# Kernel optimization log

Hardware: AMD Instinct MI355X
Metric: run time of the kernel (lower is better)

## Reference

```python
import jax, jax.numpy as jnp
import numpy as np

RMIN, RMAX, MAX_PHASE = 0.9, 1.0, 6.283


def setup_inputs() -> dict:
    key = jax.random.key(0)
    ks = jax.random.split(key, 12)
    Bsz, T, U, O, S, H = 16, 4096, 128, 128, 256, 512
    inp = jax.random.normal(ks[0], (Bsz, T, U), dtype=jnp.float32)
    # stable complex diagonal: |lambda| in [RMIN, RMAX], phase in [0, MAX_PHASE]
    r = RMIN + (RMAX - RMIN) * jax.random.uniform(ks[1], (S,), dtype=jnp.float32)
    theta = MAX_PHASE * jax.random.uniform(ks[2], (S,), dtype=jnp.float32)
    Lambda_re = r * jnp.cos(theta)
    Lambda_im = r * jnp.sin(theta)
    B = jax.random.normal(ks[3], (S, U), dtype=jnp.float32) / np.sqrt(U)
    C = jax.random.normal(ks[4], (O, S), dtype=jnp.float32) / np.sqrt(S)
    D = jax.random.normal(ks[5], (O, U), dtype=jnp.float32) / np.sqrt(U)
    W1 = jax.random.normal(ks[6], (H, O), dtype=jnp.float32) / np.sqrt(O)
    W2 = jax.random.normal(ks[7], (H, H), dtype=jnp.float32) / np.sqrt(H)
    W3 = jax.random.normal(ks[8], (O, H), dtype=jnp.float32) / np.sqrt(H)
    Wlin = jax.random.normal(ks[9], (O, U), dtype=jnp.float32) / np.sqrt(U)
    return {"input": inp, "Lambda_re": Lambda_re, "Lambda_im": Lambda_im,
            "B": B, "C": C, "D": D, "W1": W1, "W2": W2, "W3": W3, "Wlin": Wlin}


def _linear_scan(lam, bu):
    # lam: (S,) complex; bu: (B, T, S) complex
    # h_t = lam * h_{t-1} + bu_t, h_0 = 0  (work-efficient associative scan)
    A = jnp.broadcast_to(lam[None, None, :], bu.shape)

    def combine(c1, c2):
        a1, x1 = c1
        a2, x2 = c2
        return a1 * a2, a2 * x1 + x2

    _, h = jax.lax.associative_scan(combine, (A, bu), axis=1)
    return h


def reference(input, Lambda_re, Lambda_im, B, C, D, W1, W2, W3, Wlin):
    lam = (Lambda_re + 1j * Lambda_im).astype(jnp.complex64)        # (S,)
    bu = jnp.einsum('btu,su->bts', input, B).astype(jnp.complex64)   # (B,T,S)
    h = _linear_scan(lam, bu)                                        # (B,T,S) complex
    # LRU readout: real(C h) + D u
    y = jnp.einsum('bts,os->bto', h, C.astype(jnp.complex64)).real \
        + jnp.einsum('btu,ou->bto', input, D)                        # (B,T,O)
    # MLP: Linear->SiLU->Linear->ReLU->Linear (no biases)
    z = jax.nn.silu(y @ W1.T)
    z = jax.nn.relu(z @ W2.T)
    mlp_out = z @ W3.T                                               # (B,T,O)
    # residual linear path
    return mlp_out + input @ Wlin.T
```

## Files before the change

### kernel.cpp

```cpp
#include <hip/hip_runtime.h>
#include <hip/hip_bf16.h>

#define BSZ 16
#define TT 4096
#define UU 128
#define OO 128
#define SS 256
#define HH 512
#define BT (BSZ*TT)
#define CLEN 64
#define NCH (TT/CLEN)

using bf16x8 = __attribute__((ext_vector_type(8))) short;
using f32x4  = __attribute__((ext_vector_type(4))) float;

__device__ __forceinline__ unsigned short f2bf(float x){
  union { float f; unsigned int u; } v; v.f = x;
  unsigned int r = v.u + 0x7fffu + ((v.u >> 16) & 1u);
  return (unsigned short)(r >> 16);
}
__device__ __forceinline__ float bf2f(unsigned short h){
  union { float f; unsigned int u; } v; v.u = ((unsigned int)h) << 16;
  return v.f;
}

#define GLD16(g, s) __builtin_amdgcn_global_load_lds( \
    (const __attribute__((address_space(1))) unsigned int*)(g), \
    (__attribute__((address_space(3))) unsigned int*)(s), 16, 0, 0)

#define SBAR() do{ __builtin_amdgcn_sched_barrier(0); \
                   __builtin_amdgcn_s_barrier(); \
                   __builtin_amdgcn_sched_barrier(0); }while(0)

__global__ __launch_bounds__(256) void split_k(const float* __restrict__ x,
                                               unsigned short* __restrict__ H,
                                               unsigned short* __restrict__ L, int n4){
  int i = blockIdx.x * 256 + threadIdx.x;
  if (i >= n4) return;
  float4 v = ((const float4*)x)[i];
  unsigned short h0 = f2bf(v.x), h1 = f2bf(v.y), h2 = f2bf(v.z), h3 = f2bf(v.w);
  ushort4 hh = make_ushort4(h0, h1, h2, h3);
  ushort4 ll = make_ushort4(f2bf(v.x - bf2f(h0)), f2bf(v.y - bf2f(h1)),
                            f2bf(v.z - bf2f(h2)), f2bf(v.w - bf2f(h3)));
  ((ushort4*)H)[i] = hh;
  ((ushort4*)L)[i] = ll;
}

struct WJobs {
  const float* src[7];
  unsigned short* H[7];
  unsigned short* L[7];
  int end4[7];
};
__global__ __launch_bounds__(256) void split_w(WJobs j, int total4){
  int i = blockIdx.x * 256 + threadIdx.x;
  if (i >= total4) return;
  int t = 0, base = 0;
  #pragma unroll
  for (int k = 0; k < 7; k++){
    if (i >= j.end4[k]){ t = k + 1; base = j.end4[k]; }
  }
  int idx = i - base;
  float4 v = ((const float4*)j.src[t])[idx];
  unsigned short h0 = f2bf(v.x), h1 = f2bf(v.y), h2 = f2bf(v.z), h3 = f2bf(v.w);
  ushort4 hh = make_ushort4(h0, h1, h2, h3);
  ushort4 ll = make_ushort4(f2bf(v.x - bf2f(h0)), f2bf(v.y - bf2f(h1)),
                            f2bf(v.z - bf2f(h2)), f2bf(v.w - bf2f(h3)));
  ((ushort4*)j.H[t])[idx] = hh;
  ((ushort4*)j.L[t])[idx] = ll;
}

__global__ __launch_bounds__(256, 2) void gemm_split(
    const unsigned short* __restrict__ AH1, const unsigned short* __restrict__ AL1,
    const unsigned short* __restrict__ BH1, const unsigned short* __restrict__ BL1, int K1, int f1,
    const unsigned short* __restrict__ AH2, const unsigned short* __restrict__ AL2,
    const unsigned short* __restrict__ BH2, const unsigned short* __restrict__ BL2, int K2, int f2,
    unsigned short* __restrict__ outH, unsigned short* __restrict__ outL,
    float* __restrict__ outF, int Nout, int EPI,
    const float* __restrict__ lre, const float* __restrict__ lim,
    float2* __restrict__ ends)
{
  __shared__ __align__(16) unsigned short SM[32768];
  unsigned short* Ah = SM;
  unsigned short* Al = SM + 8192;
  unsigned short* Bh = SM + 16384;
  unsigned short* Bl = SM + 24576;

  const int tid = threadIdx.x;
  const int mb = blockIdx.x, nb = blockIdx.y;
  const int l = tid & 63, w = tid >> 6;
  const int wr = w >> 1, wc = w & 1;
  const int fr = l & 15, fq = l >> 4;

  f32x4 acc[4][4];
  #pragma unroll
  for (int m = 0; m < 4; m++)
    #pragma unroll
    for (int n = 0; n < 4; n++) acc[m][n] = f32x4{0.f, 0.f, 0.f, 0.f};

  const int nkt = (K1 + K2) >> 5;

  auto STAGE = [&](int buf, int kt){
    const int k0 = kt << 5;
    const unsigned short *aH, *aL, *bH, *bL; int st, kk, flg;
    if (k0 < K1){ aH = AH1; aL = AL1; bH = BH1; bL = BL1; st = K1; kk = k0; flg = f1; }
    else        { aH = AH2; aL = AL2; bH = BH2; bL = BL2; st = K2; kk = k0 - K1; flg = f2; }
    #pragma unroll
    for (int it = 0; it < 2; it++){
      int seg = tid + it * 256;
      int r = seg >> 2, c4 = seg & 3;
      int sc = (c4 ^ ((r >> 1) & 3)) << 3;
      size_t go = (size_t)(mb*128 + r) * st + kk + sc;
      size_t gb = (size_t)(nb*128 + r) * st + kk + sc;
      int lo = buf*4096 + r*32 + c4*8;
      GLD16(aH + go, Ah + lo);
      if (flg & 1) GLD16(aL + go, Al + lo);
      GLD16(bH + gb, Bh + lo);
      if (flg & 2) GLD16(bL + gb, Bl + lo);
    }
  };

  STAGE(0, 0);
  __syncthreads();

  for (int kt = 0; kt < nkt; kt++){
    const int cur = kt & 1;
    const int flg = ((kt << 5) < K1) ? f1 : f2;
    if (kt + 1 < nkt) STAGE(cur ^ 1, kt + 1);

    bf16x8 a_h[4], a_l[4], b_h[4], b_l[4];
    #pragma unroll
    for (int m = 0; m < 4; m++){
      int lra = wr*64 + m*16 + fr;
      int ra = cur*4096 + lra*32 + ((fq ^ ((lra >> 1) & 3)) << 3);
      a_h[m] = *(const bf16x8*)&Ah[ra];
      if (flg & 1) a_l[m] = *(const bf16x8*)&Al[ra];
      int lrb = wc*64 + m*16 + fr;
      int rb = cur*4096 + lrb*32 + ((fq ^ ((lrb >> 1) & 3)) << 3);
      b_h[m] = *(const bf16x8*)&Bh[rb];
      if (flg & 2) b_l[m] = *(const bf16x8*)&Bl[rb];
    }
    __builtin_amdgcn_s_setprio(1);
    #pragma unroll
    for (int m = 0; m < 4; m++)
      #pragma unroll
      for (int n = 0; n < 4; n++)
        acc[m][n] = __builtin_amdgcn_mfma_f32_16x16x32_bf16(a_h[m], b_h[n], acc[m][n], 0, 0, 0);
    if (flg & 1)
      #pragma unroll
      for (int m = 0; m < 4; m++)
        #pragma unroll
        for (int n = 0; n < 4; n++)
          acc[m][n] = __builtin_amdgcn_mfma_f32_16x16x32_bf16(a_l[m], b_h[n], acc[m][n], 0, 0, 0);
    if (flg & 2)
      #pragma unroll
      for (int m = 0; m < 4; m++)
        #pragma unroll
        for (int n = 0; n < 4; n++)
          acc[m][n] = __builtin_amdgcn_mfma_f32_16x16x32_bf16(a_h[m], b_l[n], acc[m][n], 0, 0, 0);
    __builtin_amdgcn_s_setprio(0);

    __syncthreads();
  }

  float* fl = (float*)SM;
  #pragma unroll
  for (int m = 0; m < 4; m++)
    #pragma unroll
    for (int n = 0; n < 4; n++)
      #pragma unroll
      for (int j = 0; j < 4; j++)
        fl[(wr*64 + m*16 + fq*4 + j)*128 + wc*64 + n*16 + fr] = acc[m][n][j];
  __syncthreads();
  #pragma unroll
  for (int it = 0; it < 8; it++){
    int task = tid + (it << 8);
    int rl = task >> 4, cg = task & 15;
    float4 v0 = *(const float4*)&fl[rl*128 + cg*8];
    float4 v1 = *(const float4*)&fl[rl*128 + cg*8 + 4];
    size_t o = (size_t)(mb*128 + rl) * Nout + nb*128 + cg*8;
    if (EPI == 0){
      *(float4*)(outF + o)     = v0;
      *(float4*)(outF + o + 4) = v1;
    } else {
      float xv[8] = {v0.x,v0.y,v0.z,v0.w,v1.x,v1.y,v1.z,v1.w};
      union { unsigned short us[8]; uint4 v; } ph, pl;
      #pragma unroll
      for (int e = 0; e < 8; e++){
        float x = xv[e];
        if (EPI == 2)      x = x / (1.f + __expf(-x));
        else if (EPI == 3) x = fmaxf(x, 0.f);
        ph.us[e] = f2bf(x);
        pl.us[e] = f2bf(x - bf2f(ph.us[e]));
      }
      *(uint4*)(outH + o) = ph.v;
      if (outL) *(uint4*)(outL + o) = pl.v;
    }
  }
  if (ends){
    int c = tid >> 7, sl = tid & 127;
    int b = mb >> 5, chunk = ((mb & 31) << 1) + c;
    int s = nb*128 + sl;
    float lr = lre[s], li = lim[s];
    float hr = 0.f, hi2 = 0.f;
    for (int t = 0; t < 64; t++){
      float x = fl[(c*64 + t)*128 + sl];
      float nr = fmaf(lr, hr, fmaf(-li, hi2, x));
      float ni = fmaf(lr, hi2, li * hr);
      hr = nr; hi2 = ni;
    }
    ends[((size_t)(b*NCH + chunk))*SS + s] = make_float2(hr, hi2);
  }
}

#define RING_OFF 65536

__global__ __launch_bounds__(1024, 1) void mlp_fused(
    const unsigned short* __restrict__ yH,
    const unsigned short* __restrict__ W1H,
    const unsigned short* __restrict__ W2H,
    unsigned short* __restrict__ z2H)
{
  __shared__ __align__(16) unsigned char LDS[163840];
  const int tid = threadIdx.x;
  const int l = tid & 63, w = tid >> 6;
  const int fr = l & 15, fq = l >> 4;
  const size_t r0 = (size_t)blockIdx.x * 64;

  const unsigned short* w1base[2];
  const unsigned short* w2base[2];
  int rlds[2];
  #pragma unroll
  for (int it = 0; it < 2; it++){
    int seg = l + (it << 6);
    int r = seg >> 2, c4 = seg & 3;
    int sc = (c4 ^ ((r >> 1) & 3)) << 3;
    w1base[it] = W1H + (size_t)(w*32 + r) * UU + sc;
    w2base[it] = W2H + (size_t)(w*32 + r) * HH + sc;
    rlds[it] = RING_OFF + w*6144 + seg*16;
  }
  auto stageW1 = [&](int kt){
    const int so = (kt % 3) * 2048;
    #pragma unroll
    for (int it = 0; it < 2; it++) GLD16(w1base[it] + kt*32, LDS + rlds[it] + so);
  };
  auto stageW2 = [&](int kt){
    const int so = (kt % 3) * 2048;
    #pragma unroll
    for (int it = 0; it < 2; it++) GLD16(w2base[it] + kt*32, LDS + rlds[it] + so);
  };

  {
    int r = tid >> 4, c16 = tid & 15;
    GLD16(yH + (size_t)(r0 + r) * UU + ((c16 ^ (r & 7)) << 3), LDS + tid*16);
  }
  stageW1(0);
  stageW1(1);
  asm volatile("s_waitcnt vmcnt(4)" ::: "memory");
  SBAR();

  f32x4 acc[4][2];
  #pragma unroll
  for (int m = 0; m < 4; m++)
    #pragma unroll
    for (int n = 0; n < 2; n++) acc[m][n] = f32x4{0.f, 0.f, 0.f, 0.f};

  for (int kt = 0; kt < 4; kt++){
    if (kt < 3) asm volatile("s_waitcnt vmcnt(2)" ::: "memory");
    else        asm volatile("s_waitcnt vmcnt(0)" ::: "memory");
    __builtin_amdgcn_sched_barrier(0);
    const unsigned char* Wb = LDS + RING_OFF + w*6144 + (kt % 3)*2048;
    bf16x8 a[4], b[2];
    #pragma unroll
    for (int m = 0; m < 4; m++){
      int row = m*16 + fr, kc = kt*4 + fq;
      a[m] = *(const bf16x8*)(LDS + (row*128 + ((kc ^ (row & 7)) << 3))*2);
    }
    #pragma unroll
    for (int n = 0; n < 2; n++){
      int rl = n*16 + fr;
      b[n] = *(const bf16x8*)(Wb + rl*64 + ((fq ^ ((rl >> 1) & 3)) << 4));
    }
    __builtin_amdgcn_s_setprio(1);
    #pragma unroll
    for (int m = 0; m < 4; m++)
      #pragma unroll
      for (int n = 0; n < 2; n++)
        acc[m][n] = __builtin_amdgcn_mfma_f32_16x16x32_bf16(a[m], b[n], acc[m][n], 0, 0, 0);
    __builtin_amdgcn_s_setprio(0);
    if (kt + 2 < 4) stageW1(kt + 2);
  }
  SBAR();

  stageW2(0);
  stageW2(1);

  unsigned short* Z1 = (unsigned short*)LDS;
  #pragma unroll
  for (int m = 0; m < 4; m++)
    #pragma unroll
    for (int n = 0; n < 2; n++)
      #pragma unroll
      for (int j = 0; j < 4; j++){
        float x = acc[m][n][j];
        x = x / (1.f + __expf(-x));
        int row = m*16 + fq*4 + j;
        int col = w*32 + n*16 + fr;
        Z1[(col >> 3)*512 + row*8 + (col & 7)] = f2bf(x);
      }
  SBAR();

  #pragma unroll
  for (int m = 0; m < 4; m++)
    #pragma unroll
    for (int n = 0; n < 2; n++) acc[m][n] = f32x4{0.f, 0.f, 0.f, 0.f};

  for (int kt = 0; kt < 16; kt++){
    if (kt < 15) asm volatile("s_waitcnt vmcnt(2)" ::: "memory");
    else         asm volatile("s_waitcnt vmcnt(0)" ::: "memory");
    __builtin_amdgcn_sched_barrier(0);
    const unsigned char* Wb = LDS + RING_OFF + w*6144 + (kt % 3)*2048;
    bf16x8 a[4], b[2];
    #pragma unroll
    for (int m = 0; m < 4; m++)
      a[m] = *(const bf16x8*)(LDS + (size_t)(kt*4 + fq)*1024 + (m*16 + fr)*16);
    #pragma unroll
    for (int n = 0; n < 2; n++){
      int rl = n*16 + fr;
      b[n] = *(const bf16x8*)(Wb + rl*64 + ((fq ^ ((rl >> 1) & 3)) << 4));
    }
    __builtin_amdgcn_s_setprio(1);
    #pragma unroll
    for (int m = 0; m < 4; m++)
      #pragma unroll
      for (int n = 0; n < 2; n++)
        acc[m][n] = __builtin_amdgcn_mfma_f32_16x16x32_bf16(a[m], b[n], acc[m][n], 0, 0, 0);
    __builtin_amdgcn_s_setprio(0);
    if (kt + 2 < 16) stageW2(kt + 2);
  }
  SBAR();

  unsigned short* EP = (unsigned short*)(LDS + RING_OFF);
  #pragma unroll
  for (int m = 0; m < 4; m++)
    #pragma unroll
    for (int n = 0; n < 2; n++)
      #pragma unroll
      for (int j = 0; j < 4; j++){
        float x = fmaxf(acc[m][n][j], 0.f);
        EP[(m*16 + fq*4 + j)*512 + w*32 + n*16 + fr] = f2bf(x);
      }
  __syncthreads();
  #pragma unroll
  for (int it = 0; it < 4; it++){
    int seg = tid + (it << 10);
    int r = seg >> 6, c8 = seg & 63;
    *(uint4*)(z2H + (r0 + r)*HH + c8*8) = *(const uint4*)&EP[r*512 + c8*8];
  }
}

__global__ __launch_bounds__(256) void scan_carries(const float2* __restrict__ ends,
                                                    const float* __restrict__ lre,
                                                    const float* __restrict__ lim,
                                                    float2* __restrict__ carryin){
  const int idx = blockIdx.x * 256 + threadIdx.x;
  const int b = idx >> 8;
  const int s = idx & 255;
  float pr = lre[s], pi = lim[s];
  #pragma unroll
  for (int q = 0; q < 6; q++){
    float nr = pr*pr - pi*pi;
    float ni = 2.f * pr * pi;
    pr = nr; pi = ni;
  }
  float hr = 0.f, hi = 0.f;
  for (int c = 0; c < NCH; c++){
    size_t o = ((size_t)b*NCH + c)*SS + s;
    carryin[o] = make_float2(hr, hi);
    float2 e = ends[o];
    float nr = fmaf(pr, hr, fmaf(-pi, hi, e.x));
    float ni = fmaf(pr, hi, fmaf(pi, hr, e.y));
    hr = nr; hi = ni;
  }
}

__global__ __launch_bounds__(256) void scan_apply_v(
    const unsigned short* __restrict__ buH, const unsigned short* __restrict__ buL,
    const float* __restrict__ lre, const float* __restrict__ lim,
    const float2* __restrict__ carryin, unsigned short* __restrict__ RehH){
  const int tid = threadIdx.x;
  const int grp = tid >> 6, ln = tid & 63;
  const int chunk = blockIdx.x * 4 + grp;
  const int b = chunk >> 6, ch = chunk & 63;
  const int s0 = ln * 4;
  float lr[4], li[4], hr[4], hi[4];
  #pragma unroll
  for (int e = 0; e < 4; e++){ lr[e] = lre[s0+e]; li[e] = lim[s0+e]; }
  const float2* ci = &carryin[((size_t)(b*NCH + ch))*SS + s0];
  #pragma unroll
  for (int e = 0; e < 4; e++){ hr[e] = ci[e].x; hi[e] = ci[e].y; }
  const size_t rbase = ((size_t)b*TT + (size_t)ch*CLEN)*SS + s0;
  for (int t = 0; t < CLEN; t++){
    uint2 hv = *(const uint2*)(buH + rbase + (size_t)t*SS);
    uint2 lv = *(const uint2*)(buL + rbase + (size_t)t*SS);
    const unsigned short* hs = (const unsigned short*)&hv;
    const unsigned short* ls = (const unsigned short*)&lv;
    uint2 ov; unsigned short* os = (unsigned short*)&ov;
    #pragma unroll
    for (int e = 0; e < 4; e++){
      float x = bf2f(hs[e]) + bf2f(ls[e]);
      float nr = fmaf(lr[e], hr[e], fmaf(-li[e], hi[e], x));
      float ni = fmaf(lr[e], hi[e], li[e] * hr[e]);
      hr[e] = nr; hi[e] = ni;
      os[e] = f2bf(nr);
    }
    *(uint2*)(RehH + rbase + (size_t)t*SS) = ov;
  }
}

extern "C" void kernel_launch(void* const* d_in, const int* in_sizes, int n_in,
                              void* d_out, int out_size, void* d_ws, size_t ws_size,
                              hipStream_t stream){
  const float* inp = (const float*)d_in[0];
  const float* lre = (const float*)d_in[1];
  const float* lim = (const float*)d_in[2];
  const float* Bm  = (const float*)d_in[3];
  const float* Cm  = (const float*)d_in[4];
  const float* Dm  = (const float*)d_in[5];
  const float* W1  = (const float*)d_in[6];
  const float* W2  = (const float*)d_in[7];
  const float* W3  = (const float*)d_in[8];
  const float* Wl  = (const float*)d_in[9];
  float* out = (float*)d_out;

  char* ws = (char*)d_ws;
  size_t off = 0;
  auto alloc = [&](size_t bytes)->char*{
    char* p = ws + off; off += (bytes + 255) & ~(size_t)255; return p;
  };
  unsigned short* inH  = (unsigned short*)alloc((size_t)BT*UU*2);
  unsigned short* inL  = (unsigned short*)alloc((size_t)BT*UU*2);
  char* Rbu = alloc((size_t)BT*SS*2*2);
  unsigned short* buH = (unsigned short*)Rbu;
  unsigned short* buL = (unsigned short*)(Rbu + (size_t)BT*SS*2);
  char* R2 = alloc((size_t)BT*HH*2);
  unsigned short* RehH = (unsigned short*)R2;
  unsigned short* yH   = (unsigned short*)(R2 + (size_t)BT*SS*2);
  unsigned short* z2H  = (unsigned short*)Rbu;
  unsigned short* BwH = (unsigned short*)alloc((size_t)SS*UU*2);
  unsigned short* BwL = (unsigned short*)alloc((size_t)SS*UU*2);
  unsigned short* CH_ = (unsigned short*)alloc((size_t)OO*SS*2);
  unsigned short* CL_ = (unsigned short*)alloc((size_t)OO*SS*2);
  unsigned short* DH_ = (unsigned short*)alloc((size_t)OO*UU*2);
  unsigned short* DL_ = (unsigned short*)alloc((size_t)OO*UU*2);
  unsigned short* W1H = (unsigned short*)alloc((size_t)HH*OO*2);
  unsigned short* W1L = (unsigned short*)alloc((size_t)HH*OO*2);
  unsigned short* W2H = (unsigned short*)alloc((size_t)HH*HH*2);
  unsigned short* W2L = (unsigned short*)alloc((size_t)HH*HH*2);
  unsigned short* W3H = (unsigned short*)alloc((size_t)OO*HH*2);
  unsigned short* W3L = (unsigned short*)alloc((size_t)OO*HH*2);
  unsigned short* WlH = (unsigned short*)alloc((size_t)OO*UU*2);
  unsigned short* WlL = (unsigned short*)alloc((size_t)OO*UU*2);
  float2* ends    = (float2*)alloc((size_t)BSZ*NCH*SS*8);
  float2* carryin = (float2*)alloc((size_t)BSZ*NCH*SS*8);
  if (off > ws_size) return;

  split_k<<<(BT*UU/4 + 255)/256, 256, 0, stream>>>(inp, inH, inL, BT*UU/4);
  {
    WJobs j;
    const float* srcs[7] = {Bm, Cm, Dm, W1, W2, W3, Wl};
    unsigned short* Hs[7] = {BwH, CH_, DH_, W1H, W2H, W3H, WlH};
    unsigned short* Ls[7] = {BwL, CL_, DL_, W1L, W2L, W3L, WlL};
    int n4s[7] = {SS*UU/4, OO*SS/4, OO*UU/4, HH*OO/4, HH*HH/4, OO*HH/4, OO*UU/4};
    int cum = 0;
    for (int k = 0; k < 7; k++){
      j.src[k] = srcs[k]; j.H[k] = Hs[k]; j.L[k] = Ls[k];
      cum += n4s[k]; j.end4[k] = cum;
    }
    split_w<<<(cum + 255)/256, 256, 0, stream>>>(j, cum);
  }

  gemm_split<<<dim3(BT/128, SS/128), 256, 0, stream>>>(
      inH, inL, BwH, BwL, UU, 3,
      inH, inL, BwH, BwL, 0,  3,
      buH, buL, nullptr, SS, 1,
      lre, lim, ends);

  scan_carries<<<(BSZ*SS)/256, 256, 0, stream>>>(ends, lre, lim, carryin);

  scan_apply_v<<<BSZ*NCH/4, 256, 0, stream>>>(buH, buL, lre, lim, carryin, RehH);

  gemm_split<<<dim3(BT/128, OO/128), 256, 0, stream>>>(
      RehH, RehH, CH_, CL_, SS, 2,
      inH,  inL,  DH_, DL_, UU, 3,
      yH, nullptr, nullptr, OO, 1,
      nullptr, nullptr, nullptr);

  mlp_fused<<<BT/64, 1024, 0, stream>>>(yH, W1H, W2H, z2H);

  gemm_split<<<dim3(BT/128, OO/128), 256, 0, stream>>>(
      z2H, z2H, W3H, W3L, HH, 2,
      inH, inL, WlH, WlL, UU, 3,
      nullptr, nullptr, out, OO, 0,
      nullptr, nullptr, nullptr);
}
```

Baseline: 204.8 us.

## Fuse W3 output GEMM and residual Wlin path into fused MLP kernel

Extends the fused MLP kernel to also compute the third MLP layer (z2·W3ᵀ with split-bf16 weights) and the residual input·Wlinᵀ (3-term split precision), writing fp32 output directly. This removes the z2 intermediate round trip through global memory (BT×512 bf16 write and read) and one kernel launch. The trade-off is a longer kernel per block with extra weight staging through the LDS ring, more LDS loads of the input tile, and additional barriers.

```diff
diff --git a/kernel.cpp b/kernel.cpp
--- a/kernel.cpp
+++ b/kernel.cpp
@@ -217,45 +217,51 @@
 
 __global__ __launch_bounds__(1024, 1) void mlp_fused(
     const unsigned short* __restrict__ yH,
-    const unsigned short* __restrict__ W1H,
-    const unsigned short* __restrict__ W2H,
-    unsigned short* __restrict__ z2H)
+    const unsigned short* __restrict__ inH, const unsigned short* __restrict__ inL,
+    const unsigned short* __restrict__ W1H, const unsigned short* __restrict__ W2H,
+    const unsigned short* __restrict__ W3H, const unsigned short* __restrict__ W3L,
+    const unsigned short* __restrict__ WlH, const unsigned short* __restrict__ WlL,
+    float* __restrict__ out)
 {
   __shared__ __align__(16) unsigned char LDS[163840];
   const int tid = threadIdx.x;
   const int l = tid & 63, w = tid >> 6;
   const int fr = l & 15, fq = l >> 4;
+  const int mh = w >> 3, nf = w & 7;
   const size_t r0 = (size_t)blockIdx.x * 64;
-
-  const unsigned short* w1base[2];
-  const unsigned short* w2base[2];
-  int rlds[2];
-  #pragma unroll
-  for (int it = 0; it < 2; it++){
-    int seg = l + (it << 6);
-    int r = seg >> 2, c4 = seg & 3;
-    int sc = (c4 ^ ((r >> 1) & 3)) << 3;
-    w1base[it] = W1H + (size_t)(w*32 + r) * UU + sc;
-    w2base[it] = W2H + (size_t)(w*32 + r) * HH + sc;
-    rlds[it] = RING_OFF + w*6144 + seg*16;
-  }
-  auto stageW1 = [&](int kt){
+  const int ringb = RING_OFF + w*6144;
+
+  auto stage32 = [&](const unsigned short* W, int strideK, int kt){
     const int so = (kt % 3) * 2048;
     #pragma unroll
-    for (int it = 0; it < 2; it++) GLD16(w1base[it] + kt*32, LDS + rlds[it] + so);
+    for (int it = 0; it < 2; it++){
+      int seg = l + (it << 6);
+      int r = seg >> 2, c4 = seg & 3;
+      GLD16(W + (size_t)(w*32 + r) * strideK + kt*32 + ((c4 ^ ((r >> 1) & 3)) << 3),
+            LDS + ringb + so + seg*16);
+    }
   };
-  auto stageW2 = [&](int kt){
+  auto stagePair = [&](const unsigned short* PH, const unsigned short* PL, int strideK, int kt){
     const int so = (kt % 3) * 2048;
     #pragma unroll
-    for (int it = 0; it < 2; it++) GLD16(w2base[it] + kt*32, LDS + rlds[it] + so);
+    for (int it = 0; it < 2; it++){
+      int seg = l + (it << 6);
+      const unsigned short* P = (seg >> 6) ? PL : PH;
+      int rr = (seg >> 2) & 15, c4 = seg & 3;
+      GLD16(P + (size_t)(nf*16 + rr) * strideK + kt*32 + ((c4 ^ ((rr >> 1) & 3)) << 3),
+            LDS + ringb + so + seg*16);
+    }
   };
 
   {
     int r = tid >> 4, c16 = tid & 15;
-    GLD16(yH + (size_t)(r0 + r) * UU + ((c16 ^ (r & 7)) << 3), LDS + tid*16);
-  }
-  stageW1(0);
-  stageW1(1);
+    int sc = (c16 ^ (r & 7)) << 3;
+    GLD16(yH  + (size_t)(r0 + r) * UU + sc, LDS + tid*16);
+    GLD16(inH + (size_t)(r0 + r) * UU + sc, LDS + 16384 + tid*16);
+    GLD16(inL + (size_t)(r0 + r) * UU + sc, LDS + 32768 + tid*16);
+  }
+  stage32(W1H, UU, 0);
+  stage32(W1H, UU, 1);
   asm volatile("s_waitcnt vmcnt(4)" ::: "memory");
   SBAR();
 
@@ -269,7 +275,7 @@
     if (kt < 3) asm volatile("s_waitcnt vmcnt(2)" ::: "memory");
     else        asm volatile("s_waitcnt vmcnt(0)" ::: "memory");
     __builtin_amdgcn_sched_barrier(0);
-    const unsigned char* Wb = LDS + RING_OFF + w*6144 + (kt % 3)*2048;
+    const unsigned char* Wb = LDS + ringb + (kt % 3)*2048;
     bf16x8 a[4], b[2];
     #pragma unroll
     for (int m = 0; m < 4; m++){
@@ -288,12 +294,47 @@
       for (int n = 0; n < 2; n++)
         acc[m][n] = __builtin_amdgcn_mfma_f32_16x16x32_bf16(a[m], b[n], acc[m][n], 0, 0, 0);
     __builtin_amdgcn_s_setprio(0);
-    if (kt + 2 < 4) stageW1(kt + 2);
+    if (kt + 2 < 4) stage32(W1H, UU, kt + 2);
+  }
+
+  f32x4 acc_o[2];
+  acc_o[0] = f32x4{0.f, 0.f, 0.f, 0.f};
+  acc_o[1] = f32x4{0.f, 0.f, 0.f, 0.f};
+  stagePair(WlH, WlL, UU, 0);
+  stagePair(WlH, WlL, UU, 1);
+  for (int kt = 0; kt < 4; kt++){
+    if (kt < 3) asm volatile("s_waitcnt vmcnt(2)" ::: "memory");
+    else        asm volatile("s_waitcnt vmcnt(0)" ::: "memory");
+    __builtin_amdgcn_sched_barrier(0);
+    const unsigned char* Wb = LDS + ringb + (kt % 3)*2048;
+    bf16x8 ah[2], al[2], bh, bl;
+    #pragma unroll
+    for (int m = 0; m < 2; m++){
+      int row = mh*32 + m*16 + fr, kc = kt*4 + fq;
+      int off = (row*128 + ((kc ^ (row & 7)) << 3))*2;
+      ah[m] = *(const bf16x8*)(LDS + 16384 + off);
+      al[m] = *(const bf16x8*)(LDS + 32768 + off);
+    }
+    {
+      int rl = fr;
+      int boff = rl*64 + ((fq ^ ((rl >> 1) & 3)) << 4);
+      bh = *(const bf16x8*)(Wb + boff);
+      bl = *(const bf16x8*)(Wb + 1024 + boff);
+    }
+    __builtin_amdgcn_s_setprio(1);
+    #pragma unroll
+    for (int m = 0; m < 2; m++){
+      acc_o[m] = __builtin_amdgcn_mfma_f32_16x16x32_bf16(ah[m], bh, acc_o[m], 0, 0, 0);
+      acc_o[m] = __builtin_amdgcn_mfma_f32_16x16x32_bf16(al[m], bh, acc_o[m], 0, 0, 0);
+      acc_o[m] = __builtin_amdgcn_mfma_f32_16x16x32_bf16(ah[m], bl, acc_o[m], 0, 0, 0);
+    }
+    __builtin_amdgcn_s_setprio(0);
+    if (kt + 2 < 4) stagePair(WlH, WlL, UU, kt + 2);
   }
   SBAR();
 
-  stageW2(0);
-  stageW2(1);
+  stage32(W2H, HH, 0);
+  stage32(W2H, HH, 1);
 
   unsigned short* Z1 = (unsigned short*)LDS;
   #pragma unroll
@@ -319,7 +360,7 @@
     if (kt < 15) asm volatile("s_waitcnt vmcnt(2)" ::: "memory");
     else         asm volatile("s_waitcnt vmcnt(0)" ::: "memory");
     __builtin_amdgcn_sched_barrier(0);
-    const unsigned char* Wb = LDS + RING_OFF + w*6144 + (kt % 3)*2048;
+    const unsigned char* Wb = LDS + ringb + (kt % 3)*2048;
     bf16x8 a[4], b[2];
     #pragma unroll
     for (int m = 0; m < 4; m++)
@@ -336,11 +377,14 @@
       for (int n = 0; n < 2; n++)
         acc[m][n] = __builtin_amdgcn_mfma_f32_16x16x32_bf16(a[m], b[n], acc[m][n], 0, 0, 0);
     __builtin_amdgcn_s_setprio(0);
-    if (kt + 2 < 16) stageW2(kt + 2);
-  }
+    if (kt + 2 < 16) stage32(W2H, HH, kt + 2);
+  }
+
+  stagePair(W3H, W3L, HH, 0);
+  stagePair(W3H, W3L, HH, 1);
   SBAR();
 
-  unsigned short* EP = (unsigned short*)(LDS + RING_OFF);
+  unsigned short* Z2 = (unsigned short*)LDS;
   #pragma unroll
   for (int m = 0; m < 4; m++)
     #pragma unroll
@@ -348,14 +392,50 @@
       #pragma unroll
       for (int j = 0; j < 4; j++){
         float x = fmaxf(acc[m][n][j], 0.f);
-        EP[(m*16 + fq*4 + j)*512 + w*32 + n*16 + fr] = f2bf(x);
+        int row = m*16 + fq*4 + j;
+        int col = w*32 + n*16 + fr;
+        Z2[(col >> 3)*512 + row*8 + (col & 7)] = f2bf(x);
       }
+  SBAR();
+
+  for (int kt = 0; kt < 16; kt++){
+    if (kt < 15) asm volatile("s_waitcnt vmcnt(2)" ::: "memory");
+    else         asm volatile("s_waitcnt vmcnt(0)" ::: "memory");
+    __builtin_amdgcn_sched_barrier(0);
+    const unsigned char* Wb = LDS + ringb + (kt % 3)*2048;
+    bf16x8 a[2], bh, bl;
+    #pragma unroll
+    for (int m = 0; m < 2; m++)
+      a[m] = *(const bf16x8*)(LDS + (size_t)(kt*4 + fq)*1024 + (mh*32 + m*16 + fr)*16);
+    {
+      int rl = fr;
+      int boff = rl*64 + ((fq ^ ((rl >> 1) & 3)) << 4);
+      bh = *(const bf16x8*)(Wb + boff);
+      bl = *(const bf16x8*)(Wb + 1024 + boff);
+    }
+    __builtin_amdgcn_s_setprio(1);
+    #pragma unroll
+    for (int m = 0; m < 2; m++){
+      acc_o[m] = __builtin_amdgcn_mfma_f32_16x16x32_bf16(a[m], bh, acc_o[m], 0, 0, 0);
+      acc_o[m] = __builtin_amdgcn_mfma_f32_16x16x32_bf16(a[m], bl, acc_o[m], 0, 0, 0);
+    }
+    __builtin_amdgcn_s_setprio(0);
+    if (kt + 2 < 16) stagePair(W3H, W3L, HH, kt + 2);
+  }
+  SBAR();
+
+  float* EP = (float*)(LDS + RING_OFF);
+  #pragma unroll
+  for (int m = 0; m < 2; m++)
+    #pragma unroll
+    for (int j = 0; j < 4; j++)
+      EP[(mh*32 + m*16 + fq*4 + j)*128 + nf*16 + fr] = acc_o[m][j];
   __syncthreads();
   #pragma unroll
-  for (int it = 0; it < 4; it++){
+  for (int it = 0; it < 2; it++){
     int seg = tid + (it << 10);
-    int r = seg >> 6, c8 = seg & 63;
-    *(uint4*)(z2H + (r0 + r)*HH + c8*8) = *(const uint4*)&EP[r*512 + c8*8];
+    int r = seg >> 5, c4 = seg & 31;
+    *(float4*)(out + (r0 + r)*OO + c4*4) = *(const float4*)(EP + r*128 + c4*4);
   }
 }
 
@@ -446,7 +526,6 @@
   char* R2 = alloc((size_t)BT*HH*2);
   unsigned short* RehH = (unsigned short*)R2;
   unsigned short* yH   = (unsigned short*)(R2 + (size_t)BT*SS*2);
-  unsigned short* z2H  = (unsigned short*)Rbu;
   unsigned short* BwH = (unsigned short*)alloc((size_t)SS*UU*2);
   unsigned short* BwL = (unsigned short*)alloc((size_t)SS*UU*2);
   unsigned short* CH_ = (unsigned short*)alloc((size_t)OO*SS*2);
@@ -496,11 +575,6 @@
       yH, nullptr, nullptr, OO, 1,
       nullptr, nullptr, nullptr);
 
-  mlp_fused<<<BT/64, 1024, 0, stream>>>(yH, W1H, W2H, z2H);
-
-  gemm_split<<<dim3(BT/128, OO/128), 256, 0, stream>>>(
-      z2H, z2H, W3H, W3L, HH, 2,
-      inH, inL, WlH, WlL, UU, 3,
-      nullptr, nullptr, out, OO, 0,
-      nullptr, nullptr, nullptr);
-}
+  mlp_fused<<<BT/64, 1024, 0, stream>>>(yH, inH, inL, W1H, W2H, W3H, W3L,
+                                        WlH, WlL, out);
+}
```

After: 203.6 us. No clear change (-0.6%).
